# Kernel tuning notes

Hardware: AMD Instinct MI355X
Metric: run time of the kernel (lower is better)

Reference implementation:

```python
import jax, jax.numpy as jnp
import numpy as np

B, T, C, Hh, Ww = 4, 24, 128, 48, 48
N_HEAD, D_K, D_MODEL = 16, 4, 128
D_PE = D_MODEL // N_HEAD  # 8
T_PERIOD = 1000.0


def group_norm(x, gamma, beta, groups, eps=1e-5):
    # x: (N, C) or (N, C, L); normalize over each group's channels (+ trailing dims)
    shp = x.shape
    xg = x.reshape(shp[0], groups, -1)
    mu = xg.mean(-1, keepdims=True)
    var = xg.var(-1, keepdims=True)
    xn = ((xg - mu) * jax.lax.rsqrt(var + eps)).reshape(shp)
    bshape = (1, shp[1]) + (1,) * (len(shp) - 2)
    return xn * gamma.reshape(bshape) + beta.reshape(bshape)


def _lin(k, fi, fo, std):
    kw, _ = jax.random.split(k)
    return jax.random.normal(kw, (fo, fi), jnp.float32) * std, jnp.zeros((fo,), jnp.float32)


def setup_inputs():
    key = jax.random.key(0)
    ks = jax.random.split(key, 8)
    std_k = float(np.sqrt(2.0 / D_K))
    p = {}
    p['x'] = jax.random.normal(ks[0], (B, T, C, Hh, Ww), jnp.float32)
    p['batch_positions'] = jnp.sort(jax.random.randint(ks[1], (B, T), 0, 365), axis=1).astype(jnp.int32)
    # inconv: 128 -> 256 -> 128, each Linear + GroupNorm(4) + ReLU
    p['w_in0'], p['b_in0'] = _lin(ks[2], C, 256, float(np.sqrt(2.0 / C)))
    p['g_in0'], p['be_in0'] = jnp.ones((256,), jnp.float32), jnp.zeros((256,), jnp.float32)
    p['w_in1'], p['b_in1'] = _lin(ks[3], 256, D_MODEL, float(np.sqrt(2.0 / 256)))
    p['g_in1'], p['be_in1'] = jnp.ones((D_MODEL,), jnp.float32), jnp.zeros((D_MODEL,), jnp.float32)
    # in_norm GroupNorm(16, 128)
    p['g_innorm'], p['b_innorm'] = jnp.ones((D_MODEL,), jnp.float32), jnp.zeros((D_MODEL,), jnp.float32)
    # attention: fixed query + key projection
    p['Q'] = jax.random.normal(ks[4], (N_HEAD, D_K), jnp.float32) * std_k
    p['w_k'], p['b_k'] = _lin(ks[5], D_MODEL, N_HEAD * D_K, std_k)
    # output MLP: 128 -> 256 -> 128
    p['w_m0'], p['b_m0'] = _lin(ks[6], D_MODEL, 256, float(np.sqrt(2.0 / D_MODEL)))
    p['g_m0'], p['be_m0'] = jnp.ones((256,), jnp.float32), jnp.zeros((256,), jnp.float32)
    p['w_m1'], p['b_m1'] = _lin(ks[7], 256, 128, float(np.sqrt(2.0 / 256)))
    p['g_m1'], p['be_m1'] = jnp.ones((128,), jnp.float32), jnp.zeros((128,), jnp.float32)
    # out_norm GroupNorm(16, 128)
    p['g_out'], p['b_out'] = jnp.ones((128,), jnp.float32), jnp.zeros((128,), jnp.float32)
    return p


def ltae_forward(x, pos_f, w_in0, b_in0, g_in0, be_in0, w_in1, b_in1, g_in1, be_in1,
                 g_innorm, b_innorm, Q, w_k, b_k,
                 w_m0, b_m0, g_m0, be_m0, w_m1, b_m1, g_m1, be_m1, g_out, b_out):
    Bsz, Ts, Cc, Hp, Wp = x.shape
    N = Bsz * Hp * Wp
    # (B,T,C,H,W) -> (B,H,W,T,C) -> (N, T, C): one sequence per pixel
    out = x.transpose(0, 3, 4, 1, 2).reshape(N, Ts, Cc)
    # inconv MLP on flattened tokens
    h = out.reshape(N * Ts, Cc)
    h = jax.nn.relu(group_norm(h @ w_in0.T + b_in0, g_in0, be_in0, 4))
    h = jax.nn.relu(group_norm(h @ w_in1.T + b_in1, g_in1, be_in1, 4))
    out = h.reshape(N, Ts, D_MODEL)
    # in_norm: GroupNorm(n_head) over (C, T)
    out = group_norm(out.transpose(0, 2, 1), g_innorm, b_innorm, N_HEAD).transpose(0, 2, 1)
    # positional encoding (d_model//n_head sinusoid, tiled n_head times)
    idx = jnp.arange(D_PE)
    denom = T_PERIOD ** (2.0 * (idx // 2).astype(jnp.float32) / D_PE)
    tab = pos_f[:, :, None] / denom  # (B, T, D_PE)
    tab = jnp.where(idx % 2 == 0, jnp.sin(tab), jnp.cos(tab))
    pe = jnp.tile(tab, (1, 1, N_HEAD))  # (B, T, D_MODEL)
    out = (out.reshape(Bsz, Hp * Wp, Ts, D_MODEL) + pe[:, None]).reshape(N, Ts, D_MODEL)
    # fixed-query multi-head attention
    k = (out @ w_k.T + b_k).reshape(N, Ts, N_HEAD, D_K)
    scores = jnp.einsum('hk,nthk->nht', Q, k) / jnp.sqrt(jnp.float32(D_K))
    a = jax.nn.softmax(scores, axis=-1)  # (N, H, T)
    v = out.reshape(N, Ts, N_HEAD, D_MODEL // N_HEAD)
    o = jnp.einsum('nht,nthv->nhv', a, v).reshape(N, D_MODEL)
    # output MLP + out_norm
    m = jax.nn.relu(group_norm(o @ w_m0.T + b_m0, g_m0, be_m0, 4))
    m = jax.nn.relu(group_norm(m @ w_m1.T + b_m1, g_m1, be_m1, 4))
    y = group_norm(m, g_out, b_out, N_HEAD)
    return y.reshape(Bsz, Hp, Wp, -1).transpose(0, 3, 1, 2)  # (B, C_out, H, W)


def reference(x, batch_positions, w_in0, b_in0, g_in0, be_in0, w_in1, b_in1, g_in1, be_in1,
              g_innorm, b_innorm, Q, w_k, b_k,
              w_m0, b_m0, g_m0, be_m0, w_m1, b_m1, g_m1, be_m1, g_out, b_out):
    pos_f = batch_positions.astype(jnp.float32)
    return ltae_forward(x, pos_f, w_in0, b_in0, g_in0, be_in0, w_in1, b_in1, g_in1, be_in1,
                        g_innorm, b_innorm, Q, w_k, b_k,
                        w_m0, b_m0, g_m0, be_m0, w_m1, b_m1, g_m1, be_m1, g_out, b_out)
```

## Files before the change

kernel.cpp:

```cpp
#include <hip/hip_runtime.h>
#include <math.h>

typedef _Float16 f16x8 __attribute__((ext_vector_type(8)));
typedef float f32x4 __attribute__((ext_vector_type(4)));
typedef unsigned short ushort_t;

constexpr int HWp = 2304;
constexpr float EPS = 1e-5f;

constexpr size_t M0P_OFF = 273472;
constexpr size_t M1P_OFF = 404544;
constexpr size_t OWS_OFF = 535616;

__device__ __forceinline__ int sidx(int row, int c) {
    return ((row << 8) + ((c << 1) ^ ((row & 7) << 4))) >> 1;
}

__global__ void ltae_prep(const float* __restrict__ w_in0, const float* __restrict__ w_in1,
                          const float* __restrict__ Qm, const float* __restrict__ w_k,
                          const float* __restrict__ b_k, const int* __restrict__ bpos,
                          const float* __restrict__ w_m0, const float* __restrict__ w_m1,
                          _Float16* __restrict__ w1h, _Float16* __restrict__ w1l,
                          _Float16* __restrict__ w2h, _Float16* __restrict__ w2l,
                          _Float16* __restrict__ qkBh, _Float16* __restrict__ qkBl,
                          float* __restrict__ qb2G, float* __restrict__ peG,
                          float* __restrict__ w_m0P, float* __restrict__ w_m1P) {
    int i = blockIdx.x * 256 + threadIdx.x;
    if (i < 32768) {
        float v = w_in0[i];
        _Float16 h = (_Float16)v;
        w1h[i] = h; w1l[i] = (_Float16)(v - (float)h);
    } else if (i < 65536) {
        int j = i - 32768;
        float v = w_in1[j];
        _Float16 h = (_Float16)v;
        w2h[j] = h; w2l[j] = (_Float16)(v - (float)h);
    } else if (i < 67584) {
        int j = i - 65536; int h = j >> 7, k = j & 127;
        float s = 0.f;
        #pragma unroll
        for (int dk = 0; dk < 4; dk++) s = fmaf(Qm[h * 4 + dk], w_k[(h * 4 + dk) * 128 + k], s);
        s *= 0.5f;
        _Float16 hi = (_Float16)s;
        int ks = k >> 5, lg = (k >> 3) & 3, jj = k & 7;
        int pos = ((ks * 4 + lg) * 16 + h) * 8 + jj;
        qkBh[pos] = hi; qkBl[pos] = (_Float16)(s - (float)hi);
    } else if (i < 67600) {
        int h = i - 67584;
        float s = 0.f;
        #pragma unroll
        for (int dk = 0; dk < 4; dk++) s = fmaf(Qm[h * 4 + dk], b_k[h * 4 + dk], s);
        qb2G[h] = 0.5f * s;
    } else if (i < 68368) {
        int j = i - 67600;
        int bb = j / 192, r = j - bb * 192;
        int t = r >> 3, d = r & 7;
        const float dens[4] = {1.0f, 5.623413251903491f, 31.622776601683793f, 177.82794100389228f};
        float ang = (float)bpos[bb * 24 + t] / dens[d >> 1];
        peG[j] = (d & 1) ? cosf(ang) : sinf(ang);
    } else if (i < 101136) {
        int j = i - 68368;
        int c2 = j >> 9, rem = j & 511, o = rem >> 1, jj = rem & 1;
        w_m0P[j] = w_m0[o * 128 + c2 * 2 + jj];
    } else if (i < 133904) {
        int j = i - 101136;
        int c2 = j >> 8, rem = j & 255, o = rem >> 1, jj = rem & 1;
        w_m1P[j] = w_m1[o * 256 + c2 * 2 + jj];
    }
}

__global__ __launch_bounds__(256, 3) void ltae_main(
    const float* __restrict__ x,
    const float* __restrict__ b_in0, const float* __restrict__ g_in0, const float* __restrict__ be_in0,
    const float* __restrict__ b_in1, const float* __restrict__ g_in1, const float* __restrict__ be_in1,
    const float* __restrict__ g_innorm, const float* __restrict__ b_innorm,
    const _Float16* __restrict__ w1h, const _Float16* __restrict__ w1l,
    const _Float16* __restrict__ w2h, const _Float16* __restrict__ w2l,
    const _Float16* __restrict__ qkBh, const _Float16* __restrict__ qkBl,
    const float* __restrict__ qb2G, const float* __restrict__ peG,
    float* __restrict__ o_ws)
{
    __shared__ __align__(16) ushort_t Ah[48 * 128], Al[48 * 128];
    __shared__ __align__(16) ushort_t Hh[48 * 128], Hl[48 * 128];
    __shared__ float peS[24][8];
    __shared__ float2 partS[192];

    float* scP = (float*)Hh;

    const int tid = threadIdx.x;
    const int bid = blockIdx.x;
    const int sb  = (bid & 7) * 576 + (bid >> 3);
    const int b   = sb / 1152;
    const int pixbase = (sb - b * 1152) * 2;
    const int w  = tid >> 6;
    const int l  = tid & 63;
    const int lr = l & 15;
    const int lg = l >> 4;

    if (tid < 192) peS[tid >> 3][tid & 7] = peG[b * 192 + tid];
    for (int i = tid; i < 24 * 128; i += 256) {
        int t = i >> 7, c = i & 127;
        const float* gp = x + ((size_t)((b * 24 + t) * 128 + c)) * HWp + pixbase;
        float2 v = *(const float2*)gp;
        _Float16 h0 = (_Float16)v.x;
        _Float16 h1 = (_Float16)v.y;
        int i0 = sidx(t, c), i1 = sidx(24 + t, c);
        Ah[i0] = __builtin_bit_cast(ushort_t, h0);
        Al[i0] = __builtin_bit_cast(ushort_t, (_Float16)(v.x - (float)h0));
        Ah[i1] = __builtin_bit_cast(ushort_t, h1);
        Al[i1] = __builtin_bit_cast(ushort_t, (_Float16)(v.y - (float)h1));
    }
    __syncthreads();

    f32x4 acc2[3][2];
    #pragma unroll
    for (int m = 0; m < 3; m++)
        #pragma unroll
        for (int nt = 0; nt < 2; nt++) acc2[m][nt] = f32x4{0.f, 0.f, 0.f, 0.f};

    #pragma unroll 1
    for (int half = 0; half < 2; half++) {
        f16x8 bh[2][4], bl[2][4];
        float gg[2], bb[2], bi[2];
        #pragma unroll
        for (int nt = 0; nt < 2; nt++) {
            int n = half * 128 + w * 32 + nt * 16 + lr;
            #pragma unroll
            for (int ks = 0; ks < 4; ks++) {
                bh[nt][ks] = *(const f16x8*)(w1h + n * 128 + ks * 32 + lg * 8);
                bl[nt][ks] = *(const f16x8*)(w1l + n * 128 + ks * 32 + lg * 8);
            }
            gg[nt] = g_in0[n]; bb[nt] = be_in0[n]; bi[nt] = b_in0[n];
        }
        f32x4 acc[3][2];
        #pragma unroll
        for (int m = 0; m < 3; m++)
            #pragma unroll
            for (int nt = 0; nt < 2; nt++) acc[m][nt] = f32x4{0.f, 0.f, 0.f, 0.f};
        #pragma unroll
        for (int m = 0; m < 3; m++) {
            #pragma unroll
            for (int ks = 0; ks < 4; ks++) {
                f16x8 ah = *(const f16x8*)&Ah[sidx(m * 16 + lr, ks * 32 + lg * 8)];
                f16x8 al = *(const f16x8*)&Al[sidx(m * 16 + lr, ks * 32 + lg * 8)];
                #pragma unroll
                for (int nt = 0; nt < 2; nt++) {
                    acc[m][nt] = __builtin_amdgcn_mfma_f32_16x16x32_f16(ah, bl[nt][ks], acc[m][nt], 0, 0, 0);
                    acc[m][nt] = __builtin_amdgcn_mfma_f32_16x16x32_f16(al, bh[nt][ks], acc[m][nt], 0, 0, 0);
                    acc[m][nt] = __builtin_amdgcn_mfma_f32_16x16x32_f16(ah, bh[nt][ks], acc[m][nt], 0, 0, 0);
                }
            }
        }
        float ps[3][4], ps2[3][4];
        #pragma unroll
        for (int m = 0; m < 3; m++) {
            #pragma unroll
            for (int r = 0; r < 4; r++) {
                float v0 = acc[m][0][r] + bi[0], v1 = acc[m][1][r] + bi[1];
                float s = v0 + v1, s2 = v0 * v0 + v1 * v1;
                #pragma unroll
                for (int mk = 1; mk <= 8; mk <<= 1) { s += __shfl_xor(s, mk); s2 += __shfl_xor(s2, mk); }
                ps[m][r] = s; ps2[m][r] = s2;
            }
        }
        if (lr == 0) {
            #pragma unroll
            for (int m = 0; m < 3; m++)
                #pragma unroll
                for (int r = 0; r < 4; r++)
                    partS[w * 48 + m * 16 + lg * 4 + r] = make_float2(ps[m][r], ps2[m][r]);
        }
        __syncthreads();
        #pragma unroll
        for (int m = 0; m < 3; m++) {
            #pragma unroll
            for (int r = 0; r < 4; r++) {
                float2 q = partS[(w ^ 1) * 48 + m * 16 + lg * 4 + r];
                float st = ps[m][r] + q.x, s2t = ps2[m][r] + q.y;
                float mu = st * (1.f / 64.f);
                float rs = rsqrtf(s2t * (1.f / 64.f) - mu * mu + EPS);
                int row = m * 16 + lg * 4 + r;
                #pragma unroll
                for (int nt = 0; nt < 2; nt++) {
                    float v = acc[m][nt][r] + bi[nt];
                    float hv = fmaxf(fmaf((v - mu) * rs, gg[nt], bb[nt]), 0.f);
                    _Float16 h16 = (_Float16)hv;
                    int ii = sidx(row, w * 32 + nt * 16 + lr);
                    Hh[ii] = __builtin_bit_cast(ushort_t, h16);
                    Hl[ii] = __builtin_bit_cast(ushort_t, (_Float16)(hv - (float)h16));
                }
            }
        }
        __syncthreads();

        f16x8 b2h[2][4], b2l[2][4];
        #pragma unroll
        for (int nt = 0; nt < 2; nt++) {
            int n = w * 32 + nt * 16 + lr;
            #pragma unroll
            for (int ks = 0; ks < 4; ks++) {
                b2h[nt][ks] = *(const f16x8*)(w2h + n * 256 + half * 128 + ks * 32 + lg * 8);
                b2l[nt][ks] = *(const f16x8*)(w2l + n * 256 + half * 128 + ks * 32 + lg * 8);
            }
        }
        #pragma unroll
        for (int m = 0; m < 3; m++) {
            #pragma unroll
            for (int ks = 0; ks < 4; ks++) {
                f16x8 ah = *(const f16x8*)&Hh[sidx(m * 16 + lr, ks * 32 + lg * 8)];
                f16x8 al = *(const f16x8*)&Hl[sidx(m * 16 + lr, ks * 32 + lg * 8)];
                #pragma unroll
                for (int nt = 0; nt < 2; nt++) {
                    acc2[m][nt] = __builtin_amdgcn_mfma_f32_16x16x32_f16(ah, b2l[nt][ks], acc2[m][nt], 0, 0, 0);
                    acc2[m][nt] = __builtin_amdgcn_mfma_f32_16x16x32_f16(al, b2h[nt][ks], acc2[m][nt], 0, 0, 0);
                    acc2[m][nt] = __builtin_amdgcn_mfma_f32_16x16x32_f16(ah, b2h[nt][ks], acc2[m][nt], 0, 0, 0);
                }
            }
        }
        __syncthreads();
    }

    {
        const int cA = w * 32 + lr;
        const int cB = cA + 16;
        float b2v[2]  = {b_in1[cA], b_in1[cB]};
        float g2v[2]  = {g_in1[cA], g_in1[cB]};
        float be2v[2] = {be_in1[cA], be_in1[cB]};
        float giV[2]  = {g_innorm[cA], g_innorm[cB]};
        float biV[2]  = {b_innorm[cA], b_innorm[cB]};

        float hv[3][4][2];
        #pragma unroll
        for (int m = 0; m < 3; m++) {
            #pragma unroll
            for (int r = 0; r < 4; r++) {
                float v0 = acc2[m][0][r] + b2v[0], v1 = acc2[m][1][r] + b2v[1];
                float s = v0 + v1, s2 = v0 * v0 + v1 * v1;
                #pragma unroll
                for (int mk = 1; mk <= 8; mk <<= 1) { s += __shfl_xor(s, mk); s2 += __shfl_xor(s2, mk); }
                float mu = s * (1.f / 32.f);
                float rs = rsqrtf(s2 * (1.f / 32.f) - mu * mu + EPS);
                hv[m][r][0] = fmaxf(fmaf((v0 - mu) * rs, g2v[0], be2v[0]), 0.f);
                hv[m][r][1] = fmaxf(fmaf((v1 - mu) * rs, g2v[1], be2v[1]), 0.f);
            }
        }
        float s0[2] = {0.f, 0.f}, s02[2] = {0.f, 0.f};
        float s1[2] = {0.f, 0.f}, s12[2] = {0.f, 0.f};
        #pragma unroll
        for (int m = 0; m < 3; m++) {
            #pragma unroll
            for (int r = 0; r < 4; r++) {
                int row = m * 16 + lg * 4 + r;
                #pragma unroll
                for (int nt = 0; nt < 2; nt++) {
                    float v = hv[m][r][nt];
                    if (row >= 24) { s1[nt] += v; s12[nt] += v * v; }
                    else           { s0[nt] += v; s02[nt] += v * v; }
                }
            }
        }
        #pragma unroll
        for (int nt = 0; nt < 2; nt++) {
            #pragma unroll
            for (int mk = 0; mk < 5; mk++) {
                int msk = (mk < 3) ? (1 << mk) : (2 << mk);
                s0[nt] += __shfl_xor(s0[nt], msk);  s02[nt] += __shfl_xor(s02[nt], msk);
                s1[nt] += __shfl_xor(s1[nt], msk);  s12[nt] += __shfl_xor(s12[nt], msk);
            }
        }
        float mu0[2], rs0[2], mu1[2], rs1[2];
        #pragma unroll
        for (int nt = 0; nt < 2; nt++) {
            mu0[nt] = s0[nt] * (1.f / 192.f);
            rs0[nt] = rsqrtf(s02[nt] * (1.f / 192.f) - mu0[nt] * mu0[nt] + EPS);
            mu1[nt] = s1[nt] * (1.f / 192.f);
            rs1[nt] = rsqrtf(s12[nt] * (1.f / 192.f) - mu1[nt] * mu1[nt] + EPS);
        }
        #pragma unroll
        for (int m = 0; m < 3; m++) {
            #pragma unroll
            for (int r = 0; r < 4; r++) {
                int row = m * 16 + lg * 4 + r;
                int p1 = row >= 24;
                int t = row - (p1 ? 24 : 0);
                float pe = peS[t][lr & 7];
                #pragma unroll
                for (int nt = 0; nt < 2; nt++) {
                    float mu = p1 ? mu1[nt] : mu0[nt];
                    float rs = p1 ? rs1[nt] : rs0[nt];
                    float v = fmaf((hv[m][r][nt] - mu) * rs, giV[nt], biV[nt]) + pe;
                    _Float16 h16 = (_Float16)v;
                    int ii = sidx(row, w * 32 + nt * 16 + lr);
                    Ah[ii] = __builtin_bit_cast(ushort_t, h16);
                    Al[ii] = __builtin_bit_cast(ushort_t, (_Float16)(v - (float)h16));
                }
            }
        }
    }
    __syncthreads();

    if (w < 3) {
        const int m = w;
        f16x8 qh[4], ql[4];
        #pragma unroll
        for (int ks = 0; ks < 4; ks++) {
            qh[ks] = *(const f16x8*)(qkBh + ((ks * 4 + lg) * 16 + lr) * 8);
            ql[ks] = *(const f16x8*)(qkBl + ((ks * 4 + lg) * 16 + lr) * 8);
        }
        f32x4 sacc = f32x4{0.f, 0.f, 0.f, 0.f};
        #pragma unroll
        for (int ks = 0; ks < 4; ks++) {
            f16x8 ah = *(const f16x8*)&Ah[sidx(m * 16 + lr, ks * 32 + lg * 8)];
            f16x8 al = *(const f16x8*)&Al[sidx(m * 16 + lr, ks * 32 + lg * 8)];
            sacc = __builtin_amdgcn_mfma_f32_16x16x32_f16(ah, ql[ks], sacc, 0, 0, 0);
            sacc = __builtin_amdgcn_mfma_f32_16x16x32_f16(al, qh[ks], sacc, 0, 0, 0);
            sacc = __builtin_amdgcn_mfma_f32_16x16x32_f16(ah, qh[ks], sacc, 0, 0, 0);
        }
        float qb = qb2G[lr];
        #pragma unroll
        for (int r = 0; r < 4; r++) {
            int row = m * 16 + lg * 4 + r;
            int p = row >= 24 ? 1 : 0;
            int t = row - p * 24;
            scP[(p * 16 + lr) * 24 + t] = sacc[r] + qb;
        }
    }
    __syncthreads();

    {
        const int p = w >> 1;
        int h = (w & 1) * 8 + (l >> 3), j = l & 7;
        float* sp = scP + (p * 16 + h) * 24;
        float mx = -1e30f;
        #pragma unroll
        for (int k = 0; k < 3; k++) mx = fmaxf(mx, sp[j + 8 * k]);
        mx = fmaxf(mx, __shfl_xor(mx, 1));
        mx = fmaxf(mx, __shfl_xor(mx, 2));
        mx = fmaxf(mx, __shfl_xor(mx, 4));
        float ev[3], sum = 0.f;
        #pragma unroll
        for (int k = 0; k < 3; k++) { ev[k] = __expf(sp[j + 8 * k] - mx); sum += ev[k]; }
        sum += __shfl_xor(sum, 1);
        sum += __shfl_xor(sum, 2);
        sum += __shfl_xor(sum, 4);
        float inv = 1.f / sum;
        #pragma unroll
        for (int k = 0; k < 3; k++) sp[j + 8 * k] = ev[k] * inv;
    }

    {
        const int p = w >> 1;
        int ch = (w & 1) * 64 + l;
        int h = ch >> 3;
        const float* sp = scP + (p * 16 + h) * 24;
        float s = 0.f;
        #pragma unroll
        for (int t = 0; t < 24; t++) {
            int ii = sidx(p * 24 + t, ch);
            float v = (float)__builtin_bit_cast(_Float16, Ah[ii]) +
                      (float)__builtin_bit_cast(_Float16, Al[ii]);
            s = fmaf(sp[t], v, s);
        }
        o_ws[((size_t)(b * 2304 + pixbase + p)) * 128 + ch] = s;
    }
}

__global__ __launch_bounds__(256) void ltae_mlp(
    const float* __restrict__ o_ws,
    const float* __restrict__ w_m0P, const float* __restrict__ b_m0,
    const float* __restrict__ g_m0, const float* __restrict__ be_m0,
    const float* __restrict__ w_m1P, const float* __restrict__ b_m1,
    const float* __restrict__ g_m1, const float* __restrict__ be_m1,
    const float* __restrict__ g_out, const float* __restrict__ b_out,
    float* __restrict__ out)
{
    __shared__ float ovP[8 * 128];
    __shared__ float mmP[8 * 256];
    float* ysP = ovP;

    const int tid = threadIdx.x;
    const int bid = blockIdx.x;
    const int b = bid / 288;
    const int pix8 = (bid - b * 288) * 8;

    #pragma unroll
    for (int k = 0; k < 4; k++) {
        int i = tid + (k << 8);
        ovP[i] = o_ws[((size_t)(b * 2304 + pix8)) * 128 + i];
    }
    __syncthreads();

    {
        const int o = tid;
        float acc[8];
        #pragma unroll
        for (int pp = 0; pp < 8; pp++) acc[pp] = 0.f;
        for (int c2 = 0; c2 < 64; c2++) {
            float2 w2 = *(const float2*)(w_m0P + c2 * 512 + o * 2);
            #pragma unroll
            for (int pp = 0; pp < 8; pp++) {
                float2 x2 = *(const float2*)(ovP + pp * 128 + c2 * 2);
                acc[pp] = fmaf(w2.x, x2.x, acc[pp]);
                acc[pp] = fmaf(w2.y, x2.y, acc[pp]);
            }
        }
        float bi = b_m0[o], gg = g_m0[o], bb = be_m0[o];
        #pragma unroll
        for (int pp = 0; pp < 8; pp++) {
            float v = acc[pp] + bi;
            float s = v, s2 = v * v;
            #pragma unroll
            for (int mk = 1; mk <= 32; mk <<= 1) { s += __shfl_xor(s, mk); s2 += __shfl_xor(s2, mk); }
            float mu = s * (1.f / 64.f);
            float rs = rsqrtf(s2 * (1.f / 64.f) - mu * mu + EPS);
            mmP[pp * 256 + o] = fmaxf(fmaf((v - mu) * rs, gg, bb), 0.f);
        }
    }
    __syncthreads();

    {
        const int o = tid & 127, hw = tid >> 7;
        float acc[4];
        #pragma unroll
        for (int q = 0; q < 4; q++) acc[q] = 0.f;
        for (int c2 = 0; c2 < 128; c2++) {
            float2 w2 = *(const float2*)(w_m1P + c2 * 256 + o * 2);
            #pragma unroll
            for (int q = 0; q < 4; q++) {
                float2 x2 = *(const float2*)(mmP + (hw * 4 + q) * 256 + c2 * 2);
                acc[q] = fmaf(w2.x, x2.x, acc[q]);
                acc[q] = fmaf(w2.y, x2.y, acc[q]);
            }
        }
        float bm1 = b_m1[o], gm1 = g_m1[o], bem1 = be_m1[o];
        float go = g_out[o], bo = b_out[o];
        #pragma unroll
        for (int q = 0; q < 4; q++) {
            const int pp = hw * 4 + q;
            float v = acc[q] + bm1;
            float s = v, s2 = v * v;
            #pragma unroll
            for (int mk = 1; mk <= 16; mk <<= 1) { s += __shfl_xor(s, mk); s2 += __shfl_xor(s2, mk); }
            float mu = s * (1.f / 32.f);
            float rs = rsqrtf(s2 * (1.f / 32.f) - mu * mu + EPS);
            float v2 = fmaxf(fmaf((v - mu) * rs, gm1, bem1), 0.f);
            float t1 = v2, t2 = v2 * v2;
            #pragma unroll
            for (int mk = 1; mk <= 4; mk <<= 1) { t1 += __shfl_xor(t1, mk); t2 += __shfl_xor(t2, mk); }
            float mu2 = t1 * (1.f / 8.f);
            float rs2 = rsqrtf(t2 * (1.f / 8.f) - mu2 * mu2 + EPS);
            ysP[pp * 128 + o] = fmaf((v2 - mu2) * rs2, go, bo);
        }
    }
    __syncthreads();

    {
        const int o = tid & 127, q4 = (tid >> 7) * 4;
        float4 y4;
        y4.x = ysP[(q4 + 0) * 128 + o];
        y4.y = ysP[(q4 + 1) * 128 + o];
        y4.z = ysP[(q4 + 2) * 128 + o];
        y4.w = ysP[(q4 + 3) * 128 + o];
        *(float4*)(out + ((size_t)(b * 128 + o)) * HWp + pix8 + q4) = y4;
    }
}

extern "C" void kernel_launch(void* const* d_in, const int* in_sizes, int n_in,
                              void* d_out, int out_size, void* d_ws, size_t ws_size,
                              hipStream_t stream) {
    const float* x        = (const float*)d_in[0];
    const int*   bpos     = (const int*)  d_in[1];
    const float* w_in0    = (const float*)d_in[2];
    const float* b_in0    = (const float*)d_in[3];
    const float* g_in0    = (const float*)d_in[4];
    const float* be_in0   = (const float*)d_in[5];
    const float* w_in1    = (const float*)d_in[6];
    const float* b_in1    = (const float*)d_in[7];
    const float* g_in1    = (const float*)d_in[8];
    const float* be_in1   = (const float*)d_in[9];
    const float* g_innorm = (const float*)d_in[10];
    const float* b_innorm = (const float*)d_in[11];
    const float* Qm       = (const float*)d_in[12];
    const float* w_k      = (const float*)d_in[13];
    const float* b_k      = (const float*)d_in[14];
    const float* w_m0     = (const float*)d_in[15];
    const float* b_m0     = (const float*)d_in[16];
    const float* g_m0     = (const float*)d_in[17];
    const float* be_m0    = (const float*)d_in[18];
    const float* w_m1     = (const float*)d_in[19];
    const float* b_m1     = (const float*)d_in[20];
    const float* g_m1     = (const float*)d_in[21];
    const float* be_m1    = (const float*)d_in[22];
    const float* g_out    = (const float*)d_in[23];
    const float* b_out    = (const float*)d_in[24];

    _Float16* w1h   = (_Float16*)d_ws;
    _Float16* w1l   = w1h + 32768;
    _Float16* w2h   = w1l + 32768;
    _Float16* w2l   = w2h + 32768;
    _Float16* qkBh  = (_Float16*)((char*)d_ws + 262144);
    _Float16* qkBl  = qkBh + 2048;
    float*    qb2G  = (float*)((char*)d_ws + 270336);
    float*    peG   = (float*)((char*)d_ws + 270400);
    float*    w_m0P = (float*)((char*)d_ws + M0P_OFF);
    float*    w_m1P = (float*)((char*)d_ws + M1P_OFF);
    float*    o_ws  = (float*)((char*)d_ws + OWS_OFF);

    hipLaunchKernelGGL(ltae_prep, dim3(524), dim3(256), 0, stream,
                       w_in0, w_in1, Qm, w_k, b_k, bpos, w_m0, w_m1,
                       w1h, w1l, w2h, w2l, qkBh, qkBl, qb2G, peG, w_m0P, w_m1P);

    hipLaunchKernelGGL(ltae_main, dim3(4608), dim3(256), 0, stream,
                       x,
                       b_in0, g_in0, be_in0,
                       b_in1, g_in1, be_in1,
                       g_innorm, b_innorm,
                       w1h, w1l, w2h, w2l, qkBh, qkBl, qb2G, peG,
                       o_ws);

    hipLaunchKernelGGL(ltae_mlp, dim3(1152), dim3(256), 0, stream,
                       o_ws,
                       w_m0P, b_m0, g_m0, be_m0,
                       w_m1P, b_m1, g_m1, be_m1,
                       g_out, b_out,
                       (float*)d_out);
}
```

Baseline: 317.4 us.

## Split first GEMM into four 64-channel chunks to cut registers and LDS

The fused two-layer input MLP now processes the 256 hidden channels in four chunks of 64 instead of two of 128. Each wave holds one 16-column tile instead of two, which roughly halves the B-fragment and accumulator registers. The hidden staging buffers in LDS also shrink by half, and the launch bounds are raised from 3 to 4 blocks per CU to use the freed resources. The cost is twice as many loop iterations and barriers, plus a four-way partial-sum reduction through shared memory for the group norm.

```diff
diff --git a/kernel.cpp b/kernel.cpp
--- a/kernel.cpp
+++ b/kernel.cpp
@@ -14,6 +14,9 @@
 
 __device__ __forceinline__ int sidx(int row, int c) {
     return ((row << 8) + ((c << 1) ^ ((row & 7) << 4))) >> 1;
+}
+__device__ __forceinline__ int sidx2(int row, int c) {
+    return ((row << 7) + ((c << 1) ^ ((row & 7) << 4))) >> 1;
 }
 
 __global__ void ltae_prep(const float* __restrict__ w_in0, const float* __restrict__ w_in1,
@@ -69,7 +72,7 @@
     }
 }
 
-__global__ __launch_bounds__(256, 3) void ltae_main(
+__global__ __launch_bounds__(256, 4) void ltae_main(
     const float* __restrict__ x,
     const float* __restrict__ b_in0, const float* __restrict__ g_in0, const float* __restrict__ be_in0,
     const float* __restrict__ b_in1, const float* __restrict__ g_in1, const float* __restrict__ be_in1,
@@ -81,7 +84,7 @@
     float* __restrict__ o_ws)
 {
     __shared__ __align__(16) ushort_t Ah[48 * 128], Al[48 * 128];
-    __shared__ __align__(16) ushort_t Hh[48 * 128], Hl[48 * 128];
+    __shared__ __align__(16) ushort_t Hh[48 * 64], Hl[48 * 64];
     __shared__ float peS[24][8];
     __shared__ float2 partS[192];
 
@@ -117,38 +120,31 @@
     for (int m = 0; m < 3; m++)
         #pragma unroll
         for (int nt = 0; nt < 2; nt++) acc2[m][nt] = f32x4{0.f, 0.f, 0.f, 0.f};
+    const int n2 = w * 32 + lr;
 
     #pragma unroll 1
-    for (int half = 0; half < 2; half++) {
-        f16x8 bh[2][4], bl[2][4];
-        float gg[2], bb[2], bi[2];
-        #pragma unroll
-        for (int nt = 0; nt < 2; nt++) {
-            int n = half * 128 + w * 32 + nt * 16 + lr;
-            #pragma unroll
-            for (int ks = 0; ks < 4; ks++) {
-                bh[nt][ks] = *(const f16x8*)(w1h + n * 128 + ks * 32 + lg * 8);
-                bl[nt][ks] = *(const f16x8*)(w1l + n * 128 + ks * 32 + lg * 8);
-            }
-            gg[nt] = g_in0[n]; bb[nt] = be_in0[n]; bi[nt] = b_in0[n];
-        }
-        f32x4 acc[3][2];
-        #pragma unroll
-        for (int m = 0; m < 3; m++)
-            #pragma unroll
-            for (int nt = 0; nt < 2; nt++) acc[m][nt] = f32x4{0.f, 0.f, 0.f, 0.f};
+    for (int q = 0; q < 4; q++) {
+        const int n1 = q * 64 + w * 16 + lr;
+        f16x8 bh[4], bl[4];
+        #pragma unroll
+        for (int ks = 0; ks < 4; ks++) {
+            bh[ks] = *(const f16x8*)(w1h + n1 * 128 + ks * 32 + lg * 8);
+            bl[ks] = *(const f16x8*)(w1l + n1 * 128 + ks * 32 + lg * 8);
+        }
+        const float gg = g_in0[n1], bb = be_in0[n1], bi = b_in0[n1];
+
+        f32x4 acc1[3];
+        #pragma unroll
+        for (int m = 0; m < 3; m++) acc1[m] = f32x4{0.f, 0.f, 0.f, 0.f};
         #pragma unroll
         for (int m = 0; m < 3; m++) {
             #pragma unroll
             for (int ks = 0; ks < 4; ks++) {
                 f16x8 ah = *(const f16x8*)&Ah[sidx(m * 16 + lr, ks * 32 + lg * 8)];
                 f16x8 al = *(const f16x8*)&Al[sidx(m * 16 + lr, ks * 32 + lg * 8)];
-                #pragma unroll
-                for (int nt = 0; nt < 2; nt++) {
-                    acc[m][nt] = __builtin_amdgcn_mfma_f32_16x16x32_f16(ah, bl[nt][ks], acc[m][nt], 0, 0, 0);
-                    acc[m][nt] = __builtin_amdgcn_mfma_f32_16x16x32_f16(al, bh[nt][ks], acc[m][nt], 0, 0, 0);
-                    acc[m][nt] = __builtin_amdgcn_mfma_f32_16x16x32_f16(ah, bh[nt][ks], acc[m][nt], 0, 0, 0);
-                }
+                acc1[m] = __builtin_amdgcn_mfma_f32_16x16x32_f16(ah, bl[ks], acc1[m], 0, 0, 0);
+                acc1[m] = __builtin_amdgcn_mfma_f32_16x16x32_f16(al, bh[ks], acc1[m], 0, 0, 0);
+                acc1[m] = __builtin_amdgcn_mfma_f32_16x16x32_f16(ah, bh[ks], acc1[m], 0, 0, 0);
             }
         }
         float ps[3][4], ps2[3][4];
@@ -156,8 +152,8 @@
         for (int m = 0; m < 3; m++) {
             #pragma unroll
             for (int r = 0; r < 4; r++) {
-                float v0 = acc[m][0][r] + bi[0], v1 = acc[m][1][r] + bi[1];
-                float s = v0 + v1, s2 = v0 * v0 + v1 * v1;
+                float v = acc1[m][r] + bi;
+                float s = v, s2 = v * v;
                 #pragma unroll
                 for (int mk = 1; mk <= 8; mk <<= 1) { s += __shfl_xor(s, mk); s2 += __shfl_xor(s2, mk); }
                 ps[m][r] = s; ps2[m][r] = s2;
@@ -175,40 +171,41 @@
         for (int m = 0; m < 3; m++) {
             #pragma unroll
             for (int r = 0; r < 4; r++) {
-                float2 q = partS[(w ^ 1) * 48 + m * 16 + lg * 4 + r];
-                float st = ps[m][r] + q.x, s2t = ps2[m][r] + q.y;
+                int idx = m * 16 + lg * 4 + r;
+                float st = 0.f, s2t = 0.f;
+                #pragma unroll
+                for (int j = 0; j < 4; j++) {
+                    float2 qv = partS[j * 48 + idx];
+                    st += qv.x; s2t += qv.y;
+                }
                 float mu = st * (1.f / 64.f);
                 float rs = rsqrtf(s2t * (1.f / 64.f) - mu * mu + EPS);
-                int row = m * 16 + lg * 4 + r;
-                #pragma unroll
-                for (int nt = 0; nt < 2; nt++) {
-                    float v = acc[m][nt][r] + bi[nt];
-                    float hv = fmaxf(fmaf((v - mu) * rs, gg[nt], bb[nt]), 0.f);
-                    _Float16 h16 = (_Float16)hv;
-                    int ii = sidx(row, w * 32 + nt * 16 + lr);
-                    Hh[ii] = __builtin_bit_cast(ushort_t, h16);
-                    Hl[ii] = __builtin_bit_cast(ushort_t, (_Float16)(hv - (float)h16));
-                }
+                float v = acc1[m][r] + bi;
+                float hv = fmaxf(fmaf((v - mu) * rs, gg, bb), 0.f);
+                _Float16 h16 = (_Float16)hv;
+                int ii = sidx2(idx, w * 16 + lr);
+                Hh[ii] = __builtin_bit_cast(ushort_t, h16);
+                Hl[ii] = __builtin_bit_cast(ushort_t, (_Float16)(hv - (float)h16));
             }
         }
         __syncthreads();
 
-        f16x8 b2h[2][4], b2l[2][4];
+        f16x8 b2h[2][2], b2l[2][2];
         #pragma unroll
         for (int nt = 0; nt < 2; nt++) {
-            int n = w * 32 + nt * 16 + lr;
-            #pragma unroll
-            for (int ks = 0; ks < 4; ks++) {
-                b2h[nt][ks] = *(const f16x8*)(w2h + n * 256 + half * 128 + ks * 32 + lg * 8);
-                b2l[nt][ks] = *(const f16x8*)(w2l + n * 256 + half * 128 + ks * 32 + lg * 8);
-            }
-        }
-        #pragma unroll
-        for (int m = 0; m < 3; m++) {
-            #pragma unroll
-            for (int ks = 0; ks < 4; ks++) {
-                f16x8 ah = *(const f16x8*)&Hh[sidx(m * 16 + lr, ks * 32 + lg * 8)];
-                f16x8 al = *(const f16x8*)&Hl[sidx(m * 16 + lr, ks * 32 + lg * 8)];
+            int n = n2 + nt * 16;
+            #pragma unroll
+            for (int ks = 0; ks < 2; ks++) {
+                b2h[nt][ks] = *(const f16x8*)(w2h + n * 256 + q * 64 + ks * 32 + lg * 8);
+                b2l[nt][ks] = *(const f16x8*)(w2l + n * 256 + q * 64 + ks * 32 + lg * 8);
+            }
+        }
+        #pragma unroll
+        for (int m = 0; m < 3; m++) {
+            #pragma unroll
+            for (int ks = 0; ks < 2; ks++) {
+                f16x8 ah = *(const f16x8*)&Hh[sidx2(m * 16 + lr, ks * 32 + lg * 8)];
+                f16x8 al = *(const f16x8*)&Hl[sidx2(m * 16 + lr, ks * 32 + lg * 8)];
                 #pragma unroll
                 for (int nt = 0; nt < 2; nt++) {
                     acc2[m][nt] = __builtin_amdgcn_mfma_f32_16x16x32_f16(ah, b2l[nt][ks], acc2[m][nt], 0, 0, 0);
```

Result: slower. 352.0 us (+10.9%).
